# Optimization experiments

Measured on AMD Instinct MI355X. Metric: run time of the kernel, lower is better.

Reference implementation:

```python
import jax, jax.numpy as jnp
import numpy as np

EMBED_DIM = 1280
NUM_HEADS = 16
HEAD_DIM = EMBED_DIM // NUM_HEADS  # 80
SCALE = HEAD_DIM ** -0.5
BATCH = 16
SEQ = 1024


def setup_inputs() -> dict:
    key = jax.random.key(0)
    k1, k2, k3, k4, k5 = jax.random.split(key, 5)
    return {
        "hidden_states": jax.random.normal(k1, (BATCH, SEQ, EMBED_DIM), dtype=jnp.float32),
        "w_qkv": jax.random.normal(k2, (EMBED_DIM, 3 * EMBED_DIM), dtype=jnp.float32) * (EMBED_DIM ** -0.5),
        "b_qkv": jax.random.normal(k3, (3 * EMBED_DIM,), dtype=jnp.float32) * 0.02,
        "w_proj": jax.random.normal(k4, (EMBED_DIM, EMBED_DIM), dtype=jnp.float32) * (EMBED_DIM ** -0.5),
        "b_proj": jax.random.normal(k5, (EMBED_DIM,), dtype=jnp.float32) * 0.02,
    }


def reference(hidden_states, w_qkv, b_qkv, w_proj, b_proj):
    b, s, e = hidden_states.shape
    # QKV projection: [b, s, 3e] -> [3, b, h, s, d]
    qkv = hidden_states @ w_qkv + b_qkv
    qkv = qkv.reshape(b, s, 3, NUM_HEADS, HEAD_DIM).transpose(2, 0, 3, 1, 4)
    q, k, v = qkv[0], qkv[1], qkv[2]
    # full attention matrix [b, h, s, s]
    attn = jnp.einsum("bhqd,bhkd->bhqk", q, k) * SCALE
    attn = jax.nn.softmax(attn, axis=-1)
    # dropout p=0.0 (eval): identity
    out = jnp.einsum("bhqk,bhkd->bhqd", attn, v)
    out = out.transpose(0, 2, 1, 3).reshape(b, s, e)
    return out @ w_proj + b_proj
```

## Files before the change

kernel.cpp:

```cpp
#include <hip/hip_runtime.h>

#define BATCH 16
#define SEQ   1024
#define EMBED 1280
#define NH    16
#define HD    80
#define HDP   96
#define NQKV  3840
#define MTOK  (BATCH*SEQ)
#define SCALE 0.11180339887498948f
#define LOG2E 1.4426950408889634f

#define SK_STRIDE 104
#define SV_STRIDE 72
#define SP_STRIDE 72

typedef _Float16 half8 __attribute__((ext_vector_type(8)));
typedef _Float16 half4 __attribute__((ext_vector_type(4)));
typedef float floatx4 __attribute__((ext_vector_type(4)));

#define GLD_TO_LDS(gp, lp)                                                        \
  __builtin_amdgcn_global_load_lds(                                               \
      (const __attribute__((address_space(1))) void*)(gp),                        \
      (__attribute__((address_space(3))) void*)(lp), 16, 0, 0)

__device__ __forceinline__ float rowmax16(float x) {
#define DPP_MAX(ctrl)                                                             \
  {                                                                               \
    float y = __int_as_float(                                                     \
        __builtin_amdgcn_update_dpp(0, __float_as_int(x), ctrl, 0xF, 0xF, true)); \
    x = fmaxf(x, y);                                                              \
  }
  DPP_MAX(0xB1);
  DPP_MAX(0x4E);
  DPP_MAX(0x141);
  DPP_MAX(0x140);
#undef DPP_MAX
  return x;
}

__global__ void cvt_f32_to_f16(const float4* __restrict__ in, _Float16* __restrict__ out, int n4) {
  int i = blockIdx.x * blockDim.x + threadIdx.x;
  if (i < n4) {
    float4 v = in[i];
    half4 h;
    h[0] = (_Float16)v.x; h[1] = (_Float16)v.y; h[2] = (_Float16)v.z; h[3] = (_Float16)v.w;
    *(half4*)(out + (size_t)i * 4) = h;
  }
}

template <int N>
__global__ void cvt_transpose_f16(const float* __restrict__ in, _Float16* __restrict__ out) {
  __shared__ float tile[32][33];
  const int tx = threadIdx.x & 31, ty = threadIdx.x >> 5;
  const int k0 = blockIdx.y * 32;
  const int n0 = blockIdx.x * 32;
#pragma unroll
  for (int j = 0; j < 4; ++j)
    tile[ty + 8 * j][tx] = in[(size_t)(k0 + ty + 8 * j) * N + n0 + tx];
  __syncthreads();
#pragma unroll
  for (int j = 0; j < 4; ++j)
    out[(size_t)(n0 + ty + 8 * j) * 1280 + k0 + tx] = (_Float16)tile[tx][ty + 8 * j];
}


#define STAGE_A(H, T, D)                                                           \
  do {                                                                             \
    GLD_TO_LDS(aSrc0 + (size_t)((H) * 128) * 1280 + (T) * 64,                      \
               &sA[D][((H) * 128 + wave * 16) * 64]);                              \
    GLD_TO_LDS(aSrc0 + (size_t)((H) * 128 + 8) * 1280 + (T) * 64,                  \
               &sA[D][((H) * 128 + wave * 16 + 8) * 64]);                          \
  } while (0)

#define STAGE_B(H, T, D)                                                           \
  do {                                                                             \
    GLD_TO_LDS(bSrc0 + (size_t)((H) * 128) * 1280 + (T) * 64,                      \
               &sB[D][((H) * 128 + wave * 16) * 64]);                              \
    GLD_TO_LDS(bSrc0 + (size_t)((H) * 128 + 8) * 1280 + (T) * 64,                  \
               &sB[D][((H) * 128 + wave * 16 + 8) * 64]);                          \
  } while (0)

#define LDS_FRAG(P, ROWB, FR, KK) (*(const half8*)((P) + ((ROWB) + (FR) * 16) * 64 + cofs[KK]))

#define MFMA_Q(MIB, NIB)                                                           \
  _Pragma("unroll") for (int mi = 0; mi < 4; ++mi)                                 \
    _Pragma("unroll") for (int ni = 0; ni < 2; ++ni)                               \
      _Pragma("unroll") for (int kk = 0; kk < 2; ++kk)                             \
        acc[(MIB) + mi][(NIB) + ni] = __builtin_amdgcn_mfma_f32_16x16x32_f16(      \
            af[mi][kk], bf[(NIB) + ni][kk], acc[(MIB) + mi][(NIB) + ni], 0, 0, 0)

#define GBODY2(T, D, SA, SB, VNSTR)                                                \
  {                                                                                \
    const _Float16* pA = &sA[D][0];                                                \
    const _Float16* pB = &sB[D][0];                                                \
    if (SA) { STAGE_A(0, (T) + 1, (D) ^ 1); STAGE_A(1, (T) + 1, (D) ^ 1); }        \
    _Pragma("unroll") for (int mi = 0; mi < 4; ++mi)                               \
      _Pragma("unroll") for (int kk = 0; kk < 2; ++kk)                             \
        af[mi][kk] = LDS_FRAG(pA, rA, mi, kk);                                     \
    _Pragma("unroll") for (int ni = 0; ni < 4; ++ni)                               \
      _Pragma("unroll") for (int kk = 0; kk < 2; ++kk)                             \
        bf[ni][kk] = LDS_FRAG(pB, rB, ni, kk);                                     \
    __builtin_amdgcn_s_setprio(1);                                                 \
    MFMA_Q(0, 0);                                                                  \
    MFMA_Q(0, 2);                                                                  \
    __builtin_amdgcn_s_setprio(0);                                                 \
    _Pragma("unroll") for (int mi = 0; mi < 4; ++mi)                               \
      _Pragma("unroll") for (int kk = 0; kk < 2; ++kk)                             \
        af[mi][kk] = LDS_FRAG(pA, rA, 4 + mi, kk);                                 \
    __builtin_amdgcn_s_barrier();                                                  \
    if (SB) { STAGE_B(0, (T) + 2, (D)); STAGE_B(1, (T) + 2, (D)); }                \
    __builtin_amdgcn_s_setprio(1);                                                 \
    MFMA_Q(4, 0);                                                                  \
    MFMA_Q(4, 2);                                                                  \
    __builtin_amdgcn_s_setprio(0);                                                 \
    asm volatile("s_waitcnt " VNSTR ::: "memory");                                 \
    __builtin_amdgcn_s_barrier();                                                  \
  }

template <int MODE>
__global__ __launch_bounds__(512, 2)
void gemm256(const _Float16* __restrict__ A, const _Float16* __restrict__ Bt,
             const float* __restrict__ bias,
             _Float16* __restrict__ q_pad, _Float16* __restrict__ k_pad,
             _Float16* __restrict__ v_t, float* __restrict__ outf) {
  __shared__ __align__(16) _Float16 sA[2][256 * 64];
  __shared__ __align__(16) _Float16 sB[2][256 * 64];

  const int tid = threadIdx.x;
  const int wave = tid >> 6, lane = tid & 63, quad = lane >> 4, r16 = lane & 15;
  const int wm = wave >> 2, wn = wave & 3;

  const int pid = blockIdx.x;
  const int xcd = pid & 7, local = pid >> 3;
  const int mt = xcd * 8 + (local & 7);
  const int nt = local >> 3;
  const int m0 = mt * 256, n0 = nt * 256;

  const int l8 = lane >> 3, cg = (lane & 7) ^ l8;
  const _Float16* aSrc0 = A + ((size_t)m0 + wave * 16 + l8) * 1280 + cg * 8;
  const _Float16* bSrc0 = Bt + ((size_t)n0 + wave * 16 + l8) * 1280 + cg * 8;

  const int rA = wm * 128 + r16;
  const int rB = wn * 64 + r16;
  const int cofs[2] = { ((0 + quad) ^ (r16 & 7)) * 8, ((4 + quad) ^ (r16 & 7)) * 8 };

  floatx4 acc[8][4] = {};
  half8 af[4][2], bf[4][2];

  STAGE_A(0, 0, 0); STAGE_A(1, 0, 0); STAGE_B(0, 0, 0); STAGE_B(1, 0, 0);
  STAGE_B(0, 1, 1); STAGE_B(1, 1, 1);
  asm volatile("s_waitcnt vmcnt(4)" ::: "memory");
  __builtin_amdgcn_s_barrier();

  for (int it = 0; it < 9; ++it) {
    GBODY2(2 * it, 0, true, true, "vmcnt(4)");
    GBODY2(2 * it + 1, 1, true, true, "vmcnt(4)");
  }
  GBODY2(18, 0, true, false, "vmcnt(0)");
  GBODY2(19, 1, false, false, "vmcnt(0)");

  if (MODE == 1) {
#pragma unroll
    for (int mi = 0; mi < 8; ++mi)
#pragma unroll
      for (int ni = 0; ni < 4; ++ni) {
        int n = n0 + wn * 64 + ni * 16 + r16;
        float bv = bias[n];
#pragma unroll
        for (int r = 0; r < 4; ++r) {
          int m = m0 + wm * 128 + mi * 16 + quad * 4 + r;
          outf[(size_t)m * EMBED + n] = acc[mi][ni][r] + bv;
        }
      }
  } else {
#pragma unroll
    for (int mi = 0; mi < 8; ++mi)
#pragma unroll
      for (int ni = 0; ni < 4; ++ni) {
        int n = n0 + wn * 64 + ni * 16 + r16;
        float bv = bias[n];
        int which = n / 1280;
        int rem = n - which * 1280;
        int h = rem / 80;
        int d = rem - h * 80;
        int mbase = m0 + wm * 128 + mi * 16 + quad * 4;
        int b = mbase >> 10, s = mbase & 1023;
        int bh = b * NH + h;
        if (which == 2) {
          half4 pv;
#pragma unroll
          for (int r = 0; r < 4; ++r) pv[r] = (_Float16)(acc[mi][ni][r] + bv);
          *(half4*)(v_t + ((size_t)bh * HD + d) * SEQ + s) = pv;
        } else {
          _Float16* dst = (which == 0) ? q_pad : k_pad;
#pragma unroll
          for (int r = 0; r < 4; ++r) {
            _Float16 val = (_Float16)(acc[mi][ni][r] + bv);
            dst[((size_t)bh * SEQ + (s + r)) * HDP + d] = val;
            if (d < 16) dst[((size_t)bh * SEQ + (s + r)) * HDP + 80 + d] = (_Float16)0.f;
          }
        }
      }
  }
}

__global__ __launch_bounds__(256, 2)
void attn_kernel(const _Float16* __restrict__ q_pad, const _Float16* __restrict__ k_pad,
                 const _Float16* __restrict__ v_t, _Float16* __restrict__ attn_out) {
  __shared__ __align__(16) _Float16 sK[2][64 * SK_STRIDE];
  __shared__ __align__(16) _Float16 sV[2][96 * SV_STRIDE];
  __shared__ __align__(16) _Float16 sP[4][16 * SP_STRIDE];

  const int tid = threadIdx.x;
  const int wave = tid >> 6, lane = tid & 63, quad = lane >> 4, r16 = lane & 15;
  const int bh = blockIdx.x & 255;
  const int q0 = (blockIdx.x >> 8) * 128;

  if (tid < 128) {
    int row = 80 + (tid >> 3), col = (tid & 7) * 8;
    half8 z;
#pragma unroll
    for (int j = 0; j < 8; ++j) z[j] = (row == 80) ? (_Float16)1.f : (_Float16)0.f;
    *(half8*)(&sV[0][row * SV_STRIDE + col]) = z;
    *(half8*)(&sV[1][row * SV_STRIDE + col]) = z;
  }

  half8 qf[2][3];
#pragma unroll
  for (int mi = 0; mi < 2; ++mi) {
    const _Float16* qb = q_pad + ((size_t)bh * SEQ + q0 + wave * 32 + mi * 16 + r16) * HDP;
#pragma unroll
    for (int kq = 0; kq < 3; ++kq) {
      half8 q = *(const half8*)(qb + kq * 32 + quad * 8);
#pragma unroll
      for (int j = 0; j < 8; ++j) q[j] = q[j] * (_Float16)(SCALE * LOG2E);
      qf[mi][kq] = q;
    }
  }

  int rowK[3], colK[3];
#pragma unroll
  for (int i = 0; i < 3; ++i) {
    int c = tid + i * 256;
    rowK[i] = c / 12; colK[i] = c - rowK[i] * 12;
  }
  const int rowV0 = tid >> 3, colV0 = tid & 7;
  const _Float16* kgb = k_pad + ((size_t)bh * SEQ) * HDP;
  const _Float16* vgb = v_t + (size_t)bh * HD * SEQ;

  {
    uint4 tk0 = *(const uint4*)(kgb + (size_t)(rowK[0]) * HDP + colK[0] * 8);
    uint4 tk1 = *(const uint4*)(kgb + (size_t)(rowK[1]) * HDP + colK[1] * 8);
    uint4 tk2 = *(const uint4*)(kgb + (size_t)(rowK[2]) * HDP + colK[2] * 8);
    uint4 tv0 = *(const uint4*)(vgb + (size_t)(rowV0) * SEQ + colV0 * 8);
    uint4 tv1 = *(const uint4*)(vgb + (size_t)(rowV0 + 32) * SEQ + colV0 * 8);
    *(uint4*)(&sK[0][rowK[0] * SK_STRIDE + colK[0] * 8]) = tk0;
    *(uint4*)(&sK[0][rowK[1] * SK_STRIDE + colK[1] * 8]) = tk1;
    *(uint4*)(&sK[0][rowK[2] * SK_STRIDE + colK[2] * 8]) = tk2;
    *(uint4*)(&sV[0][(rowV0)*SV_STRIDE + colV0 * 8]) = tv0;
    *(uint4*)(&sV[0][(rowV0 + 32) * SV_STRIDE + colV0 * 8]) = tv1;
    if (tid < 128) {
      uint4 tv2 = *(const uint4*)(vgb + (size_t)(rowV0 + 64) * SEQ + colV0 * 8);
      *(uint4*)(&sV[0][(rowV0 + 64) * SV_STRIDE + colV0 * 8]) = tv2;
    }
  }

  floatx4 o[2][6] = {};
  float mrow[2][4];
#pragma unroll
  for (int mi = 0; mi < 2; ++mi)
#pragma unroll
    for (int r = 0; r < 4; ++r) mrow[mi][r] = -1e30f;

  __syncthreads();

  for (int kt = 0; kt < 16; ++kt) {
    const int cur = kt & 1, nxt = cur ^ 1;

    uint4 tk0, tk1, tk2, tv0, tv1, tv2;
    if (kt < 15) {
      const int kb = (kt + 1) * 64;
      tk0 = *(const uint4*)(kgb + (size_t)(kb + rowK[0]) * HDP + colK[0] * 8);
      tk1 = *(const uint4*)(kgb + (size_t)(kb + rowK[1]) * HDP + colK[1] * 8);
      tk2 = *(const uint4*)(kgb + (size_t)(kb + rowK[2]) * HDP + colK[2] * 8);
      tv0 = *(const uint4*)(vgb + (size_t)(rowV0)*SEQ + kb + colV0 * 8);
      tv1 = *(const uint4*)(vgb + (size_t)(rowV0 + 32) * SEQ + kb + colV0 * 8);
      if (tid < 128)
        tv2 = *(const uint4*)(vgb + (size_t)(rowV0 + 64) * SEQ + kb + colV0 * 8);
    }

    floatx4 sacc[2][4] = {};
    __builtin_amdgcn_s_setprio(1);
#pragma unroll
    for (int ni = 0; ni < 4; ++ni)
#pragma unroll
      for (int kq = 0; kq < 3; ++kq) {
        half8 kf = *(const half8*)(&sK[cur][(ni * 16 + r16) * SK_STRIDE + kq * 32 + quad * 8]);
#pragma unroll
        for (int mi = 0; mi < 2; ++mi)
          sacc[mi][ni] = __builtin_amdgcn_mfma_f32_16x16x32_f16(qf[mi][kq], kf, sacc[mi][ni], 0, 0, 0);
      }
    __builtin_amdgcn_s_setprio(0);

    if (kt < 15) {
      *(uint4*)(&sK[nxt][rowK[0] * SK_STRIDE + colK[0] * 8]) = tk0;
      *(uint4*)(&sK[nxt][rowK[1] * SK_STRIDE + colK[1] * 8]) = tk1;
      *(uint4*)(&sK[nxt][rowK[2] * SK_STRIDE + colK[2] * 8]) = tk2;
      *(uint4*)(&sV[nxt][(rowV0)*SV_STRIDE + colV0 * 8]) = tv0;
      *(uint4*)(&sV[nxt][(rowV0 + 32) * SV_STRIDE + colV0 * 8]) = tv1;
      if (tid < 128)
        *(uint4*)(&sV[nxt][(rowV0 + 64) * SV_STRIDE + colV0 * 8]) = tv2;
    }

#pragma unroll
    for (int mi = 0; mi < 2; ++mi)
#pragma unroll
      for (int r = 0; r < 4; ++r) {
        float mx = fmaxf(fmaxf(sacc[mi][0][r], sacc[mi][1][r]),
                         fmaxf(sacc[mi][2][r], sacc[mi][3][r]));
        mx = rowmax16(mx);
        if (mx > mrow[mi][r]) {
          float alpha = __builtin_amdgcn_exp2f(mrow[mi][r] - mx);
          mrow[mi][r] = mx;
#pragma unroll
          for (int di = 0; di < 6; ++di) o[mi][di][r] *= alpha;
        }
        float m = mrow[mi][r];
#pragma unroll
        for (int ni = 0; ni < 4; ++ni)
          sacc[mi][ni][r] = __builtin_amdgcn_exp2f(sacc[mi][ni][r] - m);
      }

#pragma unroll
    for (int mi = 0; mi < 2; ++mi) {
#pragma unroll
      for (int ni = 0; ni < 4; ++ni)
#pragma unroll
        for (int r = 0; r < 4; ++r)
          sP[wave][(quad * 4 + r) * SP_STRIDE + ni * 16 + r16] = (_Float16)sacc[mi][ni][r];
#pragma unroll
      for (int kp = 0; kp < 2; ++kp) {
        half8 pf = *(const half8*)(&sP[wave][r16 * SP_STRIDE + kp * 32 + quad * 8]);
        __builtin_amdgcn_s_setprio(1);
#pragma unroll
        for (int di = 0; di < 6; ++di) {
          half8 vf = *(const half8*)(&sV[cur][(di * 16 + r16) * SV_STRIDE + kp * 32 + quad * 8]);
          o[mi][di] = __builtin_amdgcn_mfma_f32_16x16x32_f16(pf, vf, o[mi][di], 0, 0, 0);
        }
        __builtin_amdgcn_s_setprio(0);
      }
    }

    __syncthreads();
  }

  const int b = bh >> 4, h = bh & 15;
#pragma unroll
  for (int mi = 0; mi < 2; ++mi)
#pragma unroll
    for (int r = 0; r < 4; ++r) {
      float l = __shfl(o[mi][5][r], lane & 48);
      float inv = 1.0f / l;
      int tok = b * SEQ + q0 + wave * 32 + mi * 16 + quad * 4 + r;
#pragma unroll
      for (int di = 0; di < 5; ++di) {
        int e = h * HD + di * 16 + r16;
        attn_out[(size_t)tok * EMBED + e] = (_Float16)(o[mi][di][r] * inv);
      }
    }
}

extern "C" void kernel_launch(void* const* d_in, const int* in_sizes, int n_in,
                              void* d_out, int out_size, void* d_ws, size_t ws_size,
                              hipStream_t stream) {
  const float* hidden = (const float*)d_in[0];
  const float* w_qkv  = (const float*)d_in[1];
  const float* b_qkv  = (const float*)d_in[2];
  const float* w_proj = (const float*)d_in[3];
  const float* b_proj = (const float*)d_in[4];
  float* out = (float*)d_out;

  char* ws = (char*)d_ws;
  size_t off = 0;
  _Float16* hidden_h = (_Float16*)(ws + off); off += (size_t)MTOK * EMBED * 2;
  _Float16* wqkv_t   = (_Float16*)(ws + off); off += (size_t)NQKV * EMBED * 2;
  _Float16* wproj_t  = (_Float16*)(ws + off); off += (size_t)EMBED * EMBED * 2;
  _Float16* q_pad    = (_Float16*)(ws + off); off += (size_t)BATCH * NH * SEQ * HDP * 2;
  _Float16* k_pad    = (_Float16*)(ws + off); off += (size_t)BATCH * NH * SEQ * HDP * 2;
  _Float16* v_t      = (_Float16*)(ws + off); off += (size_t)BATCH * NH * HD * SEQ * 2;
  _Float16* attn_out = hidden_h;

  {
    int n4 = MTOK * EMBED / 4;
    cvt_f32_to_f16<<<(n4 + 255) / 256, 256, 0, stream>>>((const float4*)hidden, hidden_h, n4);
  }
  cvt_transpose_f16<NQKV><<<dim3(NQKV / 32, 1280 / 32), 256, 0, stream>>>(w_qkv, wqkv_t);
  cvt_transpose_f16<EMBED><<<dim3(EMBED / 32, 1280 / 32), 256, 0, stream>>>(w_proj, wproj_t);

  gemm256<0><<<960, 512, 0, stream>>>(hidden_h, wqkv_t, b_qkv, q_pad, k_pad, v_t, nullptr);

  attn_kernel<<<BATCH * NH * (SEQ / 128), 256, 0, stream>>>(q_pad, k_pad, v_t, attn_out);

  gemm256<1><<<320, 512, 0, stream>>>(attn_out, wproj_t, b_proj, nullptr, nullptr, nullptr, out);
}
```

Baseline: 585.1 us.

## Single-buffer K/V tiles in LDS to fit four attention blocks per CU

The attention kernel drops double-buffered K and V shared-memory tiles and uses one buffer each, roughly halving LDS use, and raises launch_bounds min blocks from 2 to 4. The next V tile is held in registers and written at the start of the following iteration. A new mid-iteration barrier, placed after the first softmax half, lets the next K tile be stored once all waves have finished QK^T. The aim is higher occupancy to hide latency, at the cost of an extra barrier per tile and a tighter VGPR budget that could cause spills.

```diff
diff --git a/kernel.cpp b/kernel.cpp
--- a/kernel.cpp
+++ b/kernel.cpp
@@ -205,11 +205,11 @@
   }
 }
 
-__global__ __launch_bounds__(256, 2)
+__global__ __launch_bounds__(256, 4)
 void attn_kernel(const _Float16* __restrict__ q_pad, const _Float16* __restrict__ k_pad,
                  const _Float16* __restrict__ v_t, _Float16* __restrict__ attn_out) {
-  __shared__ __align__(16) _Float16 sK[2][64 * SK_STRIDE];
-  __shared__ __align__(16) _Float16 sV[2][96 * SV_STRIDE];
+  __shared__ __align__(16) _Float16 sK[64 * SK_STRIDE];
+  __shared__ __align__(16) _Float16 sV[96 * SV_STRIDE];
   __shared__ __align__(16) _Float16 sP[4][16 * SP_STRIDE];
 
   const int tid = threadIdx.x;
@@ -222,8 +222,7 @@
     half8 z;
 #pragma unroll
     for (int j = 0; j < 8; ++j) z[j] = (row == 80) ? (_Float16)1.f : (_Float16)0.f;
-    *(half8*)(&sV[0][row * SV_STRIDE + col]) = z;
-    *(half8*)(&sV[1][row * SV_STRIDE + col]) = z;
+    *(half8*)(&sV[row * SV_STRIDE + col]) = z;
   }
 
   half8 qf[2][3];
@@ -249,20 +248,21 @@
   const _Float16* kgb = k_pad + ((size_t)bh * SEQ) * HDP;
   const _Float16* vgb = v_t + (size_t)bh * HD * SEQ;
 
+  uint4 tk0, tk1, tk2, tv0, tv1, tv2;
   {
-    uint4 tk0 = *(const uint4*)(kgb + (size_t)(rowK[0]) * HDP + colK[0] * 8);
-    uint4 tk1 = *(const uint4*)(kgb + (size_t)(rowK[1]) * HDP + colK[1] * 8);
-    uint4 tk2 = *(const uint4*)(kgb + (size_t)(rowK[2]) * HDP + colK[2] * 8);
-    uint4 tv0 = *(const uint4*)(vgb + (size_t)(rowV0) * SEQ + colV0 * 8);
-    uint4 tv1 = *(const uint4*)(vgb + (size_t)(rowV0 + 32) * SEQ + colV0 * 8);
-    *(uint4*)(&sK[0][rowK[0] * SK_STRIDE + colK[0] * 8]) = tk0;
-    *(uint4*)(&sK[0][rowK[1] * SK_STRIDE + colK[1] * 8]) = tk1;
-    *(uint4*)(&sK[0][rowK[2] * SK_STRIDE + colK[2] * 8]) = tk2;
-    *(uint4*)(&sV[0][(rowV0)*SV_STRIDE + colV0 * 8]) = tv0;
-    *(uint4*)(&sV[0][(rowV0 + 32) * SV_STRIDE + colV0 * 8]) = tv1;
+    tk0 = *(const uint4*)(kgb + (size_t)(rowK[0]) * HDP + colK[0] * 8);
+    tk1 = *(const uint4*)(kgb + (size_t)(rowK[1]) * HDP + colK[1] * 8);
+    tk2 = *(const uint4*)(kgb + (size_t)(rowK[2]) * HDP + colK[2] * 8);
+    tv0 = *(const uint4*)(vgb + (size_t)(rowV0) * SEQ + colV0 * 8);
+    tv1 = *(const uint4*)(vgb + (size_t)(rowV0 + 32) * SEQ + colV0 * 8);
+    *(uint4*)(&sK[rowK[0] * SK_STRIDE + colK[0] * 8]) = tk0;
+    *(uint4*)(&sK[rowK[1] * SK_STRIDE + colK[1] * 8]) = tk1;
+    *(uint4*)(&sK[rowK[2] * SK_STRIDE + colK[2] * 8]) = tk2;
+    *(uint4*)(&sV[(rowV0)*SV_STRIDE + colV0 * 8]) = tv0;
+    *(uint4*)(&sV[(rowV0 + 32) * SV_STRIDE + colV0 * 8]) = tv1;
     if (tid < 128) {
-      uint4 tv2 = *(const uint4*)(vgb + (size_t)(rowV0 + 64) * SEQ + colV0 * 8);
-      *(uint4*)(&sV[0][(rowV0 + 64) * SV_STRIDE + colV0 * 8]) = tv2;
+      tv2 = *(const uint4*)(vgb + (size_t)(rowV0 + 64) * SEQ + colV0 * 8);
+      *(uint4*)(&sV[(rowV0 + 64) * SV_STRIDE + colV0 * 8]) = tv2;
     }
   }
 
@@ -276,14 +276,20 @@
   __syncthreads();
 
   for (int kt = 0; kt < 16; ++kt) {
-    const int cur = kt & 1, nxt = cur ^ 1;
-
-    uint4 tk0, tk1, tk2, tv0, tv1, tv2;
     if (kt < 15) {
       const int kb = (kt + 1) * 64;
       tk0 = *(const uint4*)(kgb + (size_t)(kb + rowK[0]) * HDP + colK[0] * 8);
       tk1 = *(const uint4*)(kgb + (size_t)(kb + rowK[1]) * HDP + colK[1] * 8);
       tk2 = *(const uint4*)(kgb + (size_t)(kb + rowK[2]) * HDP + colK[2] * 8);
+    }
+    if (kt > 0) {
+      *(uint4*)(&sV[(rowV0)*SV_STRIDE + colV0 * 8]) = tv0;
+      *(uint4*)(&sV[(rowV0 + 32) * SV_STRIDE + colV0 * 8]) = tv1;
+      if (tid < 128)
+        *(uint4*)(&sV[(rowV0 + 64) * SV_STRIDE + colV0 * 8]) = tv2;
+    }
+    if (kt < 15) {
+      const int kb = (kt + 1) * 64;
       tv0 = *(const uint4*)(vgb + (size_t)(rowV0)*SEQ + kb + colV0 * 8);
       tv1 = *(const uint4*)(vgb + (size_t)(rowV0 + 32) * SEQ + kb + colV0 * 8);
       if (tid < 128)
@@ -296,61 +302,58 @@
     for (int ni = 0; ni < 4; ++ni)
 #pragma unroll
       for (int kq = 0; kq < 3; ++kq) {
-        half8 kf = *(const half8*)(&sK[cur][(ni * 16 + r16) * SK_STRIDE + kq * 32 + quad * 8]);
+        half8 kf = *(const half8*)(&sK[(ni * 16 + r16) * SK_STRIDE + kq * 32 + quad * 8]);
 #pragma unroll
         for (int mi = 0; mi < 2; ++mi)
           sacc[mi][ni] = __builtin_amdgcn_mfma_f32_16x16x32_f16(qf[mi][kq], kf, sacc[mi][ni], 0, 0, 0);
       }
     __builtin_amdgcn_s_setprio(0);
 
+#define SOFTMAX_MI(mi)                                                             \
+    _Pragma("unroll") for (int r = 0; r < 4; ++r) {                                \
+      float mx = fmaxf(fmaxf(sacc[mi][0][r], sacc[mi][1][r]),                      \
+                       fmaxf(sacc[mi][2][r], sacc[mi][3][r]));                     \
+      mx = rowmax16(mx);                                                           \
+      if (mx > mrow[mi][r]) {                                                      \
+        float alpha = __builtin_amdgcn_exp2f(mrow[mi][r] - mx);                    \
+        mrow[mi][r] = mx;                                                          \
+        _Pragma("unroll") for (int di = 0; di < 6; ++di) o[mi][di][r] *= alpha;    \
+      }                                                                            \
+      float m = mrow[mi][r];                                                       \
+      _Pragma("unroll") for (int ni = 0; ni < 4; ++ni)                             \
+        sacc[mi][ni][r] = __builtin_amdgcn_exp2f(sacc[mi][ni][r] - m);             \
+    }
+
+#define TRANSP_PV_MI(mi)                                                           \
+    {                                                                              \
+      _Pragma("unroll") for (int ni = 0; ni < 4; ++ni)                             \
+        _Pragma("unroll") for (int r = 0; r < 4; ++r)                              \
+          sP[wave][(quad * 4 + r) * SP_STRIDE + ni * 16 + r16] =                   \
+              (_Float16)sacc[mi][ni][r];                                           \
+      _Pragma("unroll") for (int kp = 0; kp < 2; ++kp) {                           \
+        half8 pf = *(const half8*)(&sP[wave][r16 * SP_STRIDE + kp * 32 + quad * 8]); \
+        __builtin_amdgcn_s_setprio(1);                                             \
+        _Pragma("unroll") for (int di = 0; di < 6; ++di) {                         \
+          half8 vf = *(const half8*)(&sV[(di * 16 + r16) * SV_STRIDE + kp * 32 + quad * 8]); \
+          o[mi][di] = __builtin_amdgcn_mfma_f32_16x16x32_f16(pf, vf, o[mi][di], 0, 0, 0); \
+        }                                                                          \
+        __builtin_amdgcn_s_setprio(0);                                             \
+      }                                                                            \
+    }
+
+    SOFTMAX_MI(0)
+
+    __syncthreads();
+
     if (kt < 15) {
-      *(uint4*)(&sK[nxt][rowK[0] * SK_STRIDE + colK[0] * 8]) = tk0;
-      *(uint4*)(&sK[nxt][rowK[1] * SK_STRIDE + colK[1] * 8]) = tk1;
-      *(uint4*)(&sK[nxt][rowK[2] * SK_STRIDE + colK[2] * 8]) = tk2;
-      *(uint4*)(&sV[nxt][(rowV0)*SV_STRIDE + colV0 * 8]) = tv0;
-      *(uint4*)(&sV[nxt][(rowV0 + 32) * SV_STRIDE + colV0 * 8]) = tv1;
-      if (tid < 128)
-        *(uint4*)(&sV[nxt][(rowV0 + 64) * SV_STRIDE + colV0 * 8]) = tv2;
-    }
-
-#pragma unroll
-    for (int mi = 0; mi < 2; ++mi)
-#pragma unroll
-      for (int r = 0; r < 4; ++r) {
-        float mx = fmaxf(fmaxf(sacc[mi][0][r], sacc[mi][1][r]),
-                         fmaxf(sacc[mi][2][r], sacc[mi][3][r]));
-        mx = rowmax16(mx);
-        if (mx > mrow[mi][r]) {
-          float alpha = __builtin_amdgcn_exp2f(mrow[mi][r] - mx);
-          mrow[mi][r] = mx;
-#pragma unroll
-          for (int di = 0; di < 6; ++di) o[mi][di][r] *= alpha;
-        }
-        float m = mrow[mi][r];
-#pragma unroll
-        for (int ni = 0; ni < 4; ++ni)
-          sacc[mi][ni][r] = __builtin_amdgcn_exp2f(sacc[mi][ni][r] - m);
-      }
-
-#pragma unroll
-    for (int mi = 0; mi < 2; ++mi) {
-#pragma unroll
-      for (int ni = 0; ni < 4; ++ni)
-#pragma unroll
-        for (int r = 0; r < 4; ++r)
-          sP[wave][(quad * 4 + r) * SP_STRIDE + ni * 16 + r16] = (_Float16)sacc[mi][ni][r];
-#pragma unroll
-      for (int kp = 0; kp < 2; ++kp) {
-        half8 pf = *(const half8*)(&sP[wave][r16 * SP_STRIDE + kp * 32 + quad * 8]);
-        __builtin_amdgcn_s_setprio(1);
-#pragma unroll
-        for (int di = 0; di < 6; ++di) {
-          half8 vf = *(const half8*)(&sV[cur][(di * 16 + r16) * SV_STRIDE + kp * 32 + quad * 8]);
-          o[mi][di] = __builtin_amdgcn_mfma_f32_16x16x32_f16(pf, vf, o[mi][di], 0, 0, 0);
-        }
-        __builtin_amdgcn_s_setprio(0);
-      }
-    }
+      *(uint4*)(&sK[rowK[0] * SK_STRIDE + colK[0] * 8]) = tk0;
+      *(uint4*)(&sK[rowK[1] * SK_STRIDE + colK[1] * 8]) = tk1;
+      *(uint4*)(&sK[rowK[2] * SK_STRIDE + colK[2] * 8]) = tk2;
+    }
+
+    TRANSP_PV_MI(0)
+    SOFTMAX_MI(1)
+    TRANSP_PV_MI(1)
 
     __syncthreads();
   }
```

Result: slower. 879.8 us (+50.4%).

## Transpose QK^T MFMA so row max is in-lane, single-buffer K tile

Applied to the files above, without the earlier changes.

Swaps the MFMA operand order for the score computation so each lane holds a full query row's column slice. The row max can then be taken in registers plus two cross-lane shuffles, replacing the DPP reduction. Rescale factors are broadcast via shuffle. P is written to LDS as half4 vectors instead of scalar stores, and the PV loop is reordered so both row blocks share each V fragment load. K is single-buffered with an extra barrier before the next tile is written, which halves K LDS usage but adds a sync per iteration.

```diff
diff --git a/kernel.cpp b/kernel.cpp
--- a/kernel.cpp
+++ b/kernel.cpp
@@ -23,21 +23,6 @@
   __builtin_amdgcn_global_load_lds(                                               \
       (const __attribute__((address_space(1))) void*)(gp),                        \
       (__attribute__((address_space(3))) void*)(lp), 16, 0, 0)
-
-__device__ __forceinline__ float rowmax16(float x) {
-#define DPP_MAX(ctrl)                                                             \
-  {                                                                               \
-    float y = __int_as_float(                                                     \
-        __builtin_amdgcn_update_dpp(0, __float_as_int(x), ctrl, 0xF, 0xF, true)); \
-    x = fmaxf(x, y);                                                              \
-  }
-  DPP_MAX(0xB1);
-  DPP_MAX(0x4E);
-  DPP_MAX(0x141);
-  DPP_MAX(0x140);
-#undef DPP_MAX
-  return x;
-}
 
 __global__ void cvt_f32_to_f16(const float4* __restrict__ in, _Float16* __restrict__ out, int n4) {
   int i = blockIdx.x * blockDim.x + threadIdx.x;
@@ -208,7 +193,7 @@
 __global__ __launch_bounds__(256, 2)
 void attn_kernel(const _Float16* __restrict__ q_pad, const _Float16* __restrict__ k_pad,
                  const _Float16* __restrict__ v_t, _Float16* __restrict__ attn_out) {
-  __shared__ __align__(16) _Float16 sK[2][64 * SK_STRIDE];
+  __shared__ __align__(16) _Float16 sK[64 * SK_STRIDE];
   __shared__ __align__(16) _Float16 sV[2][96 * SV_STRIDE];
   __shared__ __align__(16) _Float16 sP[4][16 * SP_STRIDE];
 
@@ -255,9 +240,9 @@
     uint4 tk2 = *(const uint4*)(kgb + (size_t)(rowK[2]) * HDP + colK[2] * 8);
     uint4 tv0 = *(const uint4*)(vgb + (size_t)(rowV0) * SEQ + colV0 * 8);
     uint4 tv1 = *(const uint4*)(vgb + (size_t)(rowV0 + 32) * SEQ + colV0 * 8);
-    *(uint4*)(&sK[0][rowK[0] * SK_STRIDE + colK[0] * 8]) = tk0;
-    *(uint4*)(&sK[0][rowK[1] * SK_STRIDE + colK[1] * 8]) = tk1;
-    *(uint4*)(&sK[0][rowK[2] * SK_STRIDE + colK[2] * 8]) = tk2;
+    *(uint4*)(&sK[rowK[0] * SK_STRIDE + colK[0] * 8]) = tk0;
+    *(uint4*)(&sK[rowK[1] * SK_STRIDE + colK[1] * 8]) = tk1;
+    *(uint4*)(&sK[rowK[2] * SK_STRIDE + colK[2] * 8]) = tk2;
     *(uint4*)(&sV[0][(rowV0)*SV_STRIDE + colV0 * 8]) = tv0;
     *(uint4*)(&sV[0][(rowV0 + 32) * SV_STRIDE + colV0 * 8]) = tv1;
     if (tid < 128) {
@@ -267,11 +252,7 @@
   }
 
   floatx4 o[2][6] = {};
-  float mrow[2][4];
-#pragma unroll
-  for (int mi = 0; mi < 2; ++mi)
-#pragma unroll
-    for (int r = 0; r < 4; ++r) mrow[mi][r] = -1e30f;
+  float mrow[2] = {-1e30f, -1e30f};
 
   __syncthreads();
 
@@ -296,17 +277,40 @@
     for (int ni = 0; ni < 4; ++ni)
 #pragma unroll
       for (int kq = 0; kq < 3; ++kq) {
-        half8 kf = *(const half8*)(&sK[cur][(ni * 16 + r16) * SK_STRIDE + kq * 32 + quad * 8]);
+        half8 kf = *(const half8*)(&sK[(ni * 16 + r16) * SK_STRIDE + kq * 32 + quad * 8]);
 #pragma unroll
         for (int mi = 0; mi < 2; ++mi)
-          sacc[mi][ni] = __builtin_amdgcn_mfma_f32_16x16x32_f16(qf[mi][kq], kf, sacc[mi][ni], 0, 0, 0);
+          sacc[mi][ni] = __builtin_amdgcn_mfma_f32_16x16x32_f16(kf, qf[mi][kq], sacc[mi][ni], 0, 0, 0);
       }
     __builtin_amdgcn_s_setprio(0);
 
+    float alphav[2];
+#pragma unroll
+    for (int mi = 0; mi < 2; ++mi) {
+      float mx = sacc[mi][0][0];
+#pragma unroll
+      for (int ni = 0; ni < 4; ++ni)
+#pragma unroll
+        for (int r = 0; r < 4; ++r) mx = fmaxf(mx, sacc[mi][ni][r]);
+      mx = fmaxf(mx, __shfl_xor(mx, 16));
+      mx = fmaxf(mx, __shfl_xor(mx, 32));
+      float a = 1.0f;
+      if (mx > mrow[mi]) { a = __builtin_amdgcn_exp2f(mrow[mi] - mx); mrow[mi] = mx; }
+      alphav[mi] = a;
+      float m = mrow[mi];
+#pragma unroll
+      for (int ni = 0; ni < 4; ++ni)
+#pragma unroll
+        for (int r = 0; r < 4; ++r)
+          sacc[mi][ni][r] = __builtin_amdgcn_exp2f(sacc[mi][ni][r] - m);
+    }
+
+    __syncthreads();
+
     if (kt < 15) {
-      *(uint4*)(&sK[nxt][rowK[0] * SK_STRIDE + colK[0] * 8]) = tk0;
-      *(uint4*)(&sK[nxt][rowK[1] * SK_STRIDE + colK[1] * 8]) = tk1;
-      *(uint4*)(&sK[nxt][rowK[2] * SK_STRIDE + colK[2] * 8]) = tk2;
+      *(uint4*)(&sK[rowK[0] * SK_STRIDE + colK[0] * 8]) = tk0;
+      *(uint4*)(&sK[rowK[1] * SK_STRIDE + colK[1] * 8]) = tk1;
+      *(uint4*)(&sK[rowK[2] * SK_STRIDE + colK[2] * 8]) = tk2;
       *(uint4*)(&sV[nxt][(rowV0)*SV_STRIDE + colV0 * 8]) = tv0;
       *(uint4*)(&sV[nxt][(rowV0 + 32) * SV_STRIDE + colV0 * 8]) = tv1;
       if (tid < 128)
@@ -317,39 +321,36 @@
     for (int mi = 0; mi < 2; ++mi)
 #pragma unroll
       for (int r = 0; r < 4; ++r) {
-        float mx = fmaxf(fmaxf(sacc[mi][0][r], sacc[mi][1][r]),
-                         fmaxf(sacc[mi][2][r], sacc[mi][3][r]));
-        mx = rowmax16(mx);
-        if (mx > mrow[mi][r]) {
-          float alpha = __builtin_amdgcn_exp2f(mrow[mi][r] - mx);
-          mrow[mi][r] = mx;
-#pragma unroll
-          for (int di = 0; di < 6; ++di) o[mi][di][r] *= alpha;
-        }
-        float m = mrow[mi][r];
-#pragma unroll
-        for (int ni = 0; ni < 4; ++ni)
-          sacc[mi][ni][r] = __builtin_amdgcn_exp2f(sacc[mi][ni][r] - m);
-      }
-
+        float ar = __shfl(alphav[mi], (lane & 48) + quad * 4 + r);
+#pragma unroll
+        for (int di = 0; di < 6; ++di) o[mi][di][r] *= ar;
+      }
+
+    half8 pf[2][2];
 #pragma unroll
     for (int mi = 0; mi < 2; ++mi) {
 #pragma unroll
-      for (int ni = 0; ni < 4; ++ni)
-#pragma unroll
-        for (int r = 0; r < 4; ++r)
-          sP[wave][(quad * 4 + r) * SP_STRIDE + ni * 16 + r16] = (_Float16)sacc[mi][ni][r];
-#pragma unroll
-      for (int kp = 0; kp < 2; ++kp) {
-        half8 pf = *(const half8*)(&sP[wave][r16 * SP_STRIDE + kp * 32 + quad * 8]);
-        __builtin_amdgcn_s_setprio(1);
-#pragma unroll
-        for (int di = 0; di < 6; ++di) {
-          half8 vf = *(const half8*)(&sV[cur][(di * 16 + r16) * SV_STRIDE + kp * 32 + quad * 8]);
-          o[mi][di] = __builtin_amdgcn_mfma_f32_16x16x32_f16(pf, vf, o[mi][di], 0, 0, 0);
-        }
-        __builtin_amdgcn_s_setprio(0);
-      }
+      for (int ni = 0; ni < 4; ++ni) {
+        half4 pp;
+#pragma unroll
+        for (int r = 0; r < 4; ++r) pp[r] = (_Float16)sacc[mi][ni][r];
+        *(half4*)(&sP[wave][r16 * SP_STRIDE + ni * 16 + quad * 4]) = pp;
+      }
+#pragma unroll
+      for (int kp = 0; kp < 2; ++kp)
+        pf[mi][kp] = *(const half8*)(&sP[wave][r16 * SP_STRIDE + kp * 32 + quad * 8]);
+    }
+
+#pragma unroll
+    for (int kp = 0; kp < 2; ++kp) {
+      __builtin_amdgcn_s_setprio(1);
+#pragma unroll
+      for (int di = 0; di < 6; ++di) {
+        half8 vf = *(const half8*)(&sV[cur][(di * 16 + r16) * SV_STRIDE + kp * 32 + quad * 8]);
+        o[0][di] = __builtin_amdgcn_mfma_f32_16x16x32_f16(pf[0][kp], vf, o[0][di], 0, 0, 0);
+        o[1][di] = __builtin_amdgcn_mfma_f32_16x16x32_f16(pf[1][kp], vf, o[1][di], 0, 0, 0);
+      }
+      __builtin_amdgcn_s_setprio(0);
     }
 
     __syncthreads();
```

New measurement: 562.8 us. 3.8% less time.
